# Kernel optimization log

Measured on AMD Instinct MI355X. Metric: run time of the kernel, lower is better.

Reference implementation:

```python
import jax, jax.numpy as jnp
import numpy as np
from jax import lax

N_SRC = 2
K_BASES = 8
N_ITER = 5
NMF_EPS = 1e-20
IP_EPS = 1e-20


def setup_inputs() -> dict:
    key = jax.random.key(0)
    kx, kt, kv = jax.random.split(key, 3)
    M, J, I = 2, 2048, 1025
    X = jax.random.normal(kx, (M, J, I, 2), dtype=jnp.float32)
    T0 = jax.random.uniform(kt, (I, K_BASES, N_SRC), dtype=jnp.float32,
                            minval=1e-08, maxval=1.0)
    V0 = jax.random.uniform(kv, (K_BASES, J, N_SRC), dtype=jnp.float32,
                            minval=1e-08, maxval=1.0)
    return {"X": X, "T0": T0, "V0": V0}


def _nmf_update(Tn, Vn, Yn, eps):
    # Tn: (I,K), Vn: (K,J), Yn: (I,J) complex
    Rn = Tn @ Vn
    magR = jnp.abs(Rn)
    YdR = jnp.abs(Yn) ** 2 / (magR ** 2 + eps)   # |Y|^2 / R^2
    Rd = 1.0 / (magR + eps)
    Tn = Tn * jnp.sqrt((YdR @ Vn.T) / (Rd @ Vn.T + eps))
    Rn = Tn @ Vn
    Rd2 = 1.0 / (jnp.abs(Rn) + eps)
    Vn = Vn * jnp.sqrt((Tn.T @ YdR) / (Tn.T @ Rd2 + eps))
    return Tn, Vn, Tn @ Vn


def _ilrma(X, T0, V0):
    M, J, I, _ = X.shape
    N = N_SRC
    # view_as_complex(X.permute(2,0,1,3)) -> (I, M, J) complex
    Xc = (X[..., 0] + 1j * X[..., 1]).astype(jnp.complex64).transpose(2, 0, 1)
    eye_M = jnp.eye(M, dtype=jnp.complex64)
    W0 = jnp.broadcast_to(jnp.eye(N, M, dtype=jnp.complex64), (I, N, M))
    Y0 = jnp.einsum('inm,imj->inj', W0, Xc)

    def one_iter(carry, _):
        W, T, V, Y = carry
        for n in range(N):  # N=2, structurally distinct small loop
            Tn, Vn, Rn = _nmf_update(T[:, :, n], V[:, :, n], Y[:, n, :], NMF_EPS)
            T = T.at[:, :, n].set(Tn)
            V = V.at[:, :, n].set(Vn)
            # batched per-frequency-bin IP update (vectorizes torch's loop over i)
            inv_Rn = 1.0 / (Rn + IP_EPS)                      # (I,J)
            Xw = Xc * jnp.sqrt(inv_Rn)[:, None, :]            # (I,M,J)
            D = jnp.einsum('imj,ikj->imk', Xw, Xw.conj()) / J  # (I,M,M)
            Dreg = D + IP_EPS * eye_M
            A = jnp.einsum('inm,imk->ink', W, Dreg)           # (I,N,M), N==M
            e_n = eye_M[:, n]                                  # (M,)
            b = jnp.linalg.solve(A, jnp.broadcast_to(e_n, (I, M))[..., None])[..., 0]  # (I,M)
            Db = jnp.einsum('imk,ik->im', Dreg, b)
            denom = jnp.sqrt(jnp.real(jnp.einsum('im,im->i', b.conj(), Db)) + IP_EPS)
            W = W.at[:, n, :].set((b / denom[:, None]).conj())
        Y = jnp.einsum('inm,imj->inj', W, Xc)
        return (W, T, V, Y), None

    (W, T, V, Y), _ = lax.scan(one_iter, (W0, T0, V0, Y0), None, length=N_ITER)
    out = Y.transpose(1, 2, 0)                 # (N, J, I)
    return jnp.stack([out.real, out.imag], axis=-1)  # view_as_real -> (N,J,I,2)


def reference(X, T0, V0):
    return _ilrma(X, T0, V0)
```

## Files before the change

kernel.cpp:

```cpp
#include <hip/hip_runtime.h>

#define I_DIM 1025
#define J_DIM 2048
#define K_B 8
#define IC 33
#define EPSF 1e-20f


__device__ __forceinline__ int rev4i(int x) {
  return ((x & 1) << 3) | ((x & 2) << 1) | ((x & 4) >> 1) | ((x & 8) >> 3);
}

__device__ __forceinline__ void foldReduce16(float* vals, int lane) {
  #pragma unroll
  for (int step = 0; step < 4; ++step) {
    const int nv = 8 >> step;
    const int bit = (lane >> step) & 1;
    #pragma unroll
    for (int q = 0; q < nv; ++q) {
      float a = vals[q], b = vals[q + nv];
      float send = bit ? a : b;
      float keep = bit ? b : a;
      vals[q] = keep + __shfl_xor(send, 1 << step);
    }
  }
  vals[0] += __shfl_xor(vals[0], 16);
  vals[0] += __shfl_xor(vals[0], 32);
}

__device__ __forceinline__ void foldReduce4(float* vals, int lane) {
  #pragma unroll
  for (int step = 0; step < 2; ++step) {
    const int nv = 2 >> step;
    const int bit = (lane >> step) & 1;
    #pragma unroll
    for (int q = 0; q < nv; ++q) {
      float a = vals[q], b = vals[q + nv];
      float send = bit ? a : b;
      float keep = bit ? b : a;
      vals[q] = keep + __shfl_xor(send, 1 << step);
    }
  }
  vals[0] += __shfl_xor(vals[0], 4);
  vals[0] += __shfl_xor(vals[0], 8);
  vals[0] += __shfl_xor(vals[0], 16);
  vals[0] += __shfl_xor(vals[0], 32);
}

__device__ __forceinline__ float2 cmul(float2 a, float2 b) {
  return make_float2(a.x*b.x - a.y*b.y, a.x*b.y + a.y*b.x);
}
__device__ __forceinline__ float2 cadd(float2 a, float2 b) {
  return make_float2(a.x + b.x, a.y + b.y);
}
__device__ __forceinline__ float2 csub(float2 a, float2 b) {
  return make_float2(a.x - b.x, a.y - b.y);
}
__device__ __forceinline__ float2 cdiv(float2 a, float2 b) {
  float s = 1.0f / (b.x*b.x + b.y*b.y);
  return make_float2((a.x*b.x + a.y*b.y)*s, (a.y*b.x - a.x*b.y)*s);
}

__global__ __launch_bounds__(256) void k_tr_init(
    const float* __restrict__ X, float4* __restrict__ Xq,
    const float* __restrict__ T0, const float* __restrict__ V0,
    float* __restrict__ T, float* __restrict__ V, float* __restrict__ W)
{
  const int tx = threadIdx.x, ty = threadIdx.y;
  const int lt = ty * 32 + tx;
  const int bid = blockIdx.y * 33 + blockIdx.x;
  int t = bid * 256 + lt;
  if (t < 2 * K_B * J_DIM) {
    int n = t >> 14;
    int r = t & 16383;
    int j = r >> 3, k = r & 7;
    V[t] = V0[(k * J_DIM + j) * 2 + n];
  }
  if (t < 2 * I_DIM * K_B) {
    int n = t / (I_DIM * K_B);
    int r = t % (I_DIM * K_B);
    int i = r / K_B, k = r % K_B;
    T[t] = T0[(i * K_B + k) * 2 + n];
  }
  if (t < I_DIM * 8) {
    int u = t & 7;
    int c = u & 1, m = (u >> 1) & 1, n = u >> 2;
    W[t] = (n == m && c == 0) ? 1.0f : 0.0f;
  }
  __shared__ float t0r[32][33], t0i[32][33], t1r[32][33], t1i[32][33];
  const int i0 = blockIdx.x * 32, j0 = blockIdx.y * 32;
  const float2* __restrict__ X2 = (const float2*)X;
  #pragma unroll
  for (int jj = 0; jj < 4; ++jj) {
    int jl = ty + jj * 8;
    int i = i0 + tx;
    if (i < I_DIM) {
      float2 v0 = X2[(size_t)(0 * J_DIM + j0 + jl) * I_DIM + i];
      float2 v1 = X2[(size_t)(1 * J_DIM + j0 + jl) * I_DIM + i];
      t0r[jl][tx] = v0.x; t0i[jl][tx] = v0.y;
      t1r[jl][tx] = v1.x; t1i[jl][tx] = v1.y;
    }
  }
  __syncthreads();
  #pragma unroll
  for (int ii = 0; ii < 4; ++ii) {
    int il = ty + ii * 8;
    int i = i0 + il;
    if (i < I_DIM) {
      Xq[(size_t)i * J_DIM + j0 + tx] =
        make_float4(t0r[tx][il], t0i[tx][il], t1r[tx][il], t1i[tx][il]);
    }
  }
}

template<int N>
__device__ __forceinline__ void nmfT_body(
    int i, int tid,
    const float4* __restrict__ Xq,
    float* __restrict__ T, const float* __restrict__ V,
    const float* __restrict__ W, float* __restrict__ YdR)
{
  float4 xs[8];
  #pragma unroll
  for (int u = 0; u < 8; ++u) xs[u] = Xq[(size_t)i * J_DIM + u * 256 + tid];

  const float4 w = ((const float4*)W)[i * 2 + N];
  float t[K_B];
  const int trow = (N * I_DIM + i) * K_B;
  #pragma unroll
  for (int k = 0; k < K_B; ++k) t[k] = T[trow + k];

  float num[K_B], den[K_B];
  #pragma unroll
  for (int k = 0; k < K_B; ++k) { num[k] = 0.f; den[k] = 0.f; }

  const float4* __restrict__ V4 = (const float4*)V;
  #pragma unroll
  for (int u = 0; u < 8; ++u) {
    int j = u * 256 + tid;
    float4 va = V4[(N * J_DIM + j) * 2 + 0];
    float4 vb = V4[(N * J_DIM + j) * 2 + 1];
    float v[K_B] = {va.x, va.y, va.z, va.w, vb.x, vb.y, vb.z, vb.w};
    float rn = 0.f;
    #pragma unroll
    for (int k = 0; k < K_B; ++k) rn += t[k] * v[k];
    float4 x = xs[u];
    float yr = w.x * x.x - w.y * x.y + w.z * x.z - w.w * x.w;
    float yi = w.x * x.y + w.y * x.x + w.z * x.w + w.w * x.z;
    float rd = 1.0f / (fabsf(rn) + EPSF);
    float ydr = (yr * yr + yi * yi) * rd * rd;
    YdR[(size_t)i * J_DIM + j] = ydr;
    #pragma unroll
    for (int k = 0; k < K_B; ++k) { num[k] += ydr * v[k]; den[k] += rd * v[k]; }
  }

  float vals[16];
  #pragma unroll
  for (int k = 0; k < K_B; ++k) { vals[k] = num[k]; vals[K_B + k] = den[k]; }
  const int wave = tid >> 6, lane = tid & 63;
  foldReduce16(vals, lane);
  __shared__ float redT[4][16];
  if (lane < 16) redT[wave][lane] = vals[0];
  __syncthreads();
  if (tid < K_B) {
    int r = rev4i(tid);
    float nm = redT[0][r] + redT[1][r] + redT[2][r] + redT[3][r];
    float dn = redT[0][r+1] + redT[1][r+1] + redT[2][r+1] + redT[3][r+1];
    T[trow + tid] *= sqrtf(nm / (dn + EPSF));
  }
}

template<int N>
__device__ __forceinline__ void ip_solve(
    int i, float D00, float p, float q, float D11, float* __restrict__ W)
{
  D00 += EPSF; D11 += EPSF;
  float2 D01 = make_float2(p, q);
  float2 D10 = make_float2(p, -q);
  float4 w0 = ((const float4*)W)[i * 2 + 0];
  float4 w1 = ((const float4*)W)[i * 2 + 1];
  float2 W00 = make_float2(w0.x, w0.y), W01 = make_float2(w0.z, w0.w);
  float2 W10 = make_float2(w1.x, w1.y), W11 = make_float2(w1.z, w1.w);
  float2 A00 = cadd(make_float2(W00.x * D00, W00.y * D00), cmul(W01, D10));
  float2 A01 = cadd(cmul(W00, D01), make_float2(W01.x * D11, W01.y * D11));
  float2 A10 = cadd(make_float2(W10.x * D00, W10.y * D00), cmul(W11, D10));
  float2 A11 = cadd(cmul(W10, D01), make_float2(W11.x * D11, W11.y * D11));
  float2 det = csub(cmul(A00, A11), cmul(A01, A10));
  float2 b0, b1;
  if (N == 0) {
    b0 = cdiv(A11, det);
    b1 = cdiv(make_float2(-A10.x, -A10.y), det);
  } else {
    b0 = cdiv(make_float2(-A01.x, -A01.y), det);
    b1 = cdiv(A00, det);
  }
  float2 Db0 = cadd(make_float2(D00 * b0.x, D00 * b0.y), cmul(D01, b1));
  float2 Db1 = cadd(cmul(D10, b0), make_float2(D11 * b1.x, D11 * b1.y));
  float ip = b0.x * Db0.x + b0.y * Db0.y + b1.x * Db1.x + b1.y * Db1.y;
  float inv = 1.0f / sqrtf(ip + EPSF);
  ((float4*)W)[i * 2 + N] = make_float4(b0.x * inv, -b0.y * inv, b1.x * inv, -b1.y * inv);
}

template<int N>
__device__ __forceinline__ void ip_body(
    int i, int tid,
    const float4* __restrict__ Xq,
    const float* __restrict__ T, const float* __restrict__ V,
    float* __restrict__ W)
{
  float4 xs[8];
  #pragma unroll
  for (int u = 0; u < 8; ++u) xs[u] = Xq[(size_t)i * J_DIM + u * 256 + tid];

  float t[K_B];
  const int trow = (N * I_DIM + i) * K_B;
  #pragma unroll
  for (int k = 0; k < K_B; ++k) t[k] = T[trow + k];

  const float4* __restrict__ V4 = (const float4*)V;
  float d00 = 0.f, d01r = 0.f, d01i = 0.f, d11 = 0.f;
  #pragma unroll
  for (int u = 0; u < 8; ++u) {
    int j = u * 256 + tid;
    float4 va = V4[(N * J_DIM + j) * 2 + 0];
    float4 vb = V4[(N * J_DIM + j) * 2 + 1];
    float rn = t[0]*va.x + t[1]*va.y + t[2]*va.z + t[3]*va.w
             + t[4]*vb.x + t[5]*vb.y + t[6]*vb.z + t[7]*vb.w;
    float wgt = 1.0f / (rn + EPSF);
    float4 x = xs[u];
    d00 += (x.x * x.x + x.y * x.y) * wgt;
    d11 += (x.z * x.z + x.w * x.w) * wgt;
    d01r += (x.x * x.z + x.y * x.w) * wgt;
    d01i += (x.y * x.z - x.x * x.w) * wgt;
  }
  float vals[4] = {d00, d01r, d01i, d11};
  const int wave = tid >> 6, lane = tid & 63;
  foldReduce4(vals, lane);
  __shared__ float redI[4][4];
  if (lane < 4) redI[wave][lane] = vals[0];
  __syncthreads();
  if (tid == 0) {
    const float invJ = 1.0f / (float)J_DIM;
    float D00 = (redI[0][0] + redI[1][0] + redI[2][0] + redI[3][0]) * invJ;
    float pr  = (redI[0][2] + redI[1][2] + redI[2][2] + redI[3][2]) * invJ;
    float qi  = (redI[0][1] + redI[1][1] + redI[2][1] + redI[3][1]) * invJ;
    float D11 = (redI[0][3] + redI[1][3] + redI[2][3] + redI[3][3]) * invJ;
    ip_solve<N>(i, D00, pr, qi, D11, W);
  }
}

template<int N>
__device__ __forceinline__ void part_body(
    int pb, int tid,
    const float* __restrict__ T, const float* __restrict__ V,
    const float* __restrict__ YdR,
    float* __restrict__ Pn, float* __restrict__ Pd)
{
  const int jb = pb & 7;
  const int c  = pb >> 3;
  const int j  = jb * 256 + tid;
  const int i0 = c * 32;
  const int ni = min(32, I_DIM - i0);
  __shared__ float sT[32 * K_B];
  if (tid < ni * K_B) sT[tid] = T[(N * I_DIM + i0) * K_B + tid];
  __syncthreads();
  const float4* __restrict__ V4 = (const float4*)V;
  float4 va = V4[(N * J_DIM + j) * 2 + 0];
  float4 vb = V4[(N * J_DIM + j) * 2 + 1];
  float v[K_B] = {va.x, va.y, va.z, va.w, vb.x, vb.y, vb.z, vb.w};
  float num[K_B], den[K_B];
  #pragma unroll
  for (int k = 0; k < K_B; ++k) { num[k] = 0.f; den[k] = 0.f; }

  if (ni == 32) {
    #pragma unroll
    for (int g = 0; g < 4; ++g) {
      float yd[8];
      #pragma unroll
      for (int q = 0; q < 8; ++q)
        yd[q] = YdR[(size_t)(i0 + g * 8 + q) * J_DIM + j];
      #pragma unroll
      for (int q = 0; q < 8; ++q) {
        const int ii = g * 8 + q;
        float rn = 0.f;
        #pragma unroll
        for (int k = 0; k < K_B; ++k) rn += sT[ii * K_B + k] * v[k];
        float rd2 = 1.0f / (fabsf(rn) + EPSF);
        #pragma unroll
        for (int k = 0; k < K_B; ++k) {
          num[k] += sT[ii * K_B + k] * yd[q];
          den[k] += sT[ii * K_B + k] * rd2;
        }
      }
    }
  } else {
    for (int ii = 0; ii < ni; ++ii) {
      float ydr = YdR[(size_t)(i0 + ii) * J_DIM + j];
      float rn = 0.f;
      #pragma unroll
      for (int k = 0; k < K_B; ++k) rn += sT[ii * K_B + k] * v[k];
      float rd2 = 1.0f / (fabsf(rn) + EPSF);
      #pragma unroll
      for (int k = 0; k < K_B; ++k) {
        num[k] += sT[ii * K_B + k] * ydr;
        den[k] += sT[ii * K_B + k] * rd2;
      }
    }
  }
  ((float4*)Pn)[((size_t)c * J_DIM + j) * 2 + 0] = make_float4(num[0], num[1], num[2], num[3]);
  ((float4*)Pn)[((size_t)c * J_DIM + j) * 2 + 1] = make_float4(num[4], num[5], num[6], num[7]);
  ((float4*)Pd)[((size_t)c * J_DIM + j) * 2 + 0] = make_float4(den[0], den[1], den[2], den[3]);
  ((float4*)Pd)[((size_t)c * J_DIM + j) * 2 + 1] = make_float4(den[4], den[5], den[6], den[7]);
}

template<int N>
__device__ __forceinline__ void fin_body(
    int fb, int tid, float* __restrict__ V,
    const float* __restrict__ Pn, const float* __restrict__ Pd)
{
  const int t = fb * 256 + tid;
  float nm = 0.f, dn = 0.f;
  #pragma unroll
  for (int c = 0; c < IC; ++c) {
    nm += Pn[(size_t)c * (K_B * J_DIM) + t];
    dn += Pd[(size_t)c * (K_B * J_DIM) + t];
  }
  V[N * (K_B * J_DIM) + t] *= sqrtf(nm / (dn + EPSF));
}

template<int NT, int NP>
__global__ __launch_bounds__(256) void k_s2(
    const float4* __restrict__ Xq, float* __restrict__ T,
    const float* __restrict__ V, const float* __restrict__ W,
    float* __restrict__ YdR_t, const float* __restrict__ YdR_p,
    float* __restrict__ Pn, float* __restrict__ Pd)
{
  if (blockIdx.x < 264)
    part_body<NP>(blockIdx.x, threadIdx.x, T, V, YdR_p, Pn, Pd);
  else
    nmfT_body<NT>(blockIdx.x - 264, threadIdx.x, Xq, T, V, W, YdR_t);
}

template<int NF, int NP>
__global__ __launch_bounds__(256) void k_s3(
    float* __restrict__ V,
    const float* __restrict__ Pn_f, const float* __restrict__ Pd_f,
    const float* __restrict__ T, const float* __restrict__ YdR_p,
    float* __restrict__ Pn_p, float* __restrict__ Pd_p)
{
  if (blockIdx.x < 64)
    fin_body<NF>(blockIdx.x, threadIdx.x, V, Pn_f, Pd_f);
  else
    part_body<NP>(blockIdx.x - 64, threadIdx.x, T, V, YdR_p, Pn_p, Pd_p);
}

template<int NI, int NF>
__global__ __launch_bounds__(256) void k_s4(
    const float4* __restrict__ Xq, const float* __restrict__ T,
    float* __restrict__ V, float* __restrict__ W,
    const float* __restrict__ Pn_f, const float* __restrict__ Pd_f)
{
  if (blockIdx.x < 64)
    fin_body<NF>(blockIdx.x, threadIdx.x, V, Pn_f, Pd_f);
  else
    ip_body<NI>(blockIdx.x - 64, threadIdx.x, Xq, T, V, W);
}

template<int NT, int NI>
__global__ __launch_bounds__(256) void k_s1(
    const float4* __restrict__ Xq, float* __restrict__ T,
    const float* __restrict__ V, float* __restrict__ W,
    float* __restrict__ YdR_t)
{
  int b = blockIdx.x;
  int p, pop;
  if (b >= 2048) { p = 1024; pop = b - 2048; }
  else { pop = (b >> 3) & 1; p = ((b >> 4) << 3) | (b & 7); }
  if (pop == 0)
    ip_body<NI>(p, threadIdx.x, Xq, T, V, W);
  else
    nmfT_body<NT>(p, threadIdx.x, Xq, T, V, W, YdR_t);
}

template<int N>
__global__ __launch_bounds__(256) void k_nmfT(
    const float4* __restrict__ Xq, float* __restrict__ T,
    const float* __restrict__ V, const float* __restrict__ W,
    float* __restrict__ YdR)
{
  nmfT_body<N>(blockIdx.x, threadIdx.x, Xq, T, V, W, YdR);
}

template<int N>
__global__ __launch_bounds__(256) void k_ip(
    const float4* __restrict__ Xq, const float* __restrict__ T,
    const float* __restrict__ V, float* __restrict__ W)
{
  ip_body<N>(blockIdx.x, threadIdx.x, Xq, T, V, W);
}

__global__ __launch_bounds__(256) void k_out(
    const float* __restrict__ X, const float* __restrict__ W, float* __restrict__ out)
{
  const int j = blockIdx.x;
  const int i = blockIdx.y * 256 + threadIdx.x;
  if (i >= I_DIM) return;
  const float2* __restrict__ X2 = (const float2*)X;
  float2 x0 = X2[(size_t)(0 * J_DIM + j) * I_DIM + i];
  float2 x1 = X2[(size_t)(1 * J_DIM + j) * I_DIM + i];
  const float4* __restrict__ W4 = (const float4*)W;
  float4 w0 = W4[i * 2 + 0];
  float4 w1 = W4[i * 2 + 1];
  float2* __restrict__ O = (float2*)out;
  float yr = w0.x * x0.x - w0.y * x0.y + w0.z * x1.x - w0.w * x1.y;
  float yi = w0.x * x0.y + w0.y * x0.x + w0.z * x1.y + w0.w * x1.x;
  O[(size_t)(0 * J_DIM + j) * I_DIM + i] = make_float2(yr, yi);
  yr = w1.x * x0.x - w1.y * x0.y + w1.z * x1.x - w1.w * x1.y;
  yi = w1.x * x0.y + w1.y * x0.x + w1.z * x1.y + w1.w * x1.x;
  O[(size_t)(1 * J_DIM + j) * I_DIM + i] = make_float2(yr, yi);
}

extern "C" void kernel_launch(void* const* d_in, const int* in_sizes, int n_in,
                              void* d_out, int out_size, void* d_ws, size_t ws_size,
                              hipStream_t stream) {
  const float* X  = (const float*)d_in[0];
  const float* T0 = (const float*)d_in[1];
  const float* V0 = (const float*)d_in[2];
  float* ws = (float*)d_ws;
  float4* Xq  = (float4*)ws;
  float* YdR0 = ws + 8396800;
  float* YdR1 = ws + 10496000;
  float* T    = ws + 12595200;
  float* V    = ws + 12611600;
  float* W    = ws + 12644368;
  float* Pn0  = ws + 12652568;
  float* Pd0  = ws + 13193240;
  float* Pn1  = ws + 13733912;
  float* Pd1  = ws + 14274584;
  float* out  = (float*)d_out;

  k_tr_init<<<dim3(33, 64), dim3(32, 8), 0, stream>>>(X, Xq, T0, V0, T, V, W);
  k_nmfT<0><<<I_DIM, 256, 0, stream>>>(Xq, T, V, W, YdR0);
  for (int it = 0; it < 5; ++it) {
    k_s2<1, 0><<<264 + I_DIM, 256, 0, stream>>>(Xq, T, V, W, YdR1, YdR0, Pn0, Pd0);
    k_s3<0, 1><<<64 + 264, 256, 0, stream>>>(V, Pn0, Pd0, T, YdR1, Pn1, Pd1);
    k_s4<0, 1><<<64 + I_DIM, 256, 0, stream>>>(Xq, T, V, W, Pn1, Pd1);
    if (it < 4) {
      k_s1<0, 1><<<2 * I_DIM, 256, 0, stream>>>(Xq, T, V, W, YdR0);
    } else {
      k_ip<1><<<I_DIM, 256, 0, stream>>>(Xq, T, V, W);
    }
  }
  k_out<<<dim3(J_DIM, 5), 256, 0, stream>>>(X, W, out);
}
```

Measured before the change: 313.4 us.

## Batch both sources per stage and fuse the two IP updates into one kernel

The staggered per-source pipeline, which interleaved the NMF, partial-sum, finalize and IP stages of sources 0 and 1 across launches, is replaced by one stage-per-kernel schedule handling both sources together. The IP kernel now loads X once per frequency bin, accumulates the weighted covariance for both sources, and solves both W rows sequentially in one thread. This removes a second full pass over X per iteration and the separate initial NMF launch. In exchange it loses the overlap between stages of different sources, and the partial-sum and finalize launches now have small grids that may underfill the GPU.

```diff
diff --git a/kernel.cpp b/kernel.cpp
--- a/kernel.cpp
+++ b/kernel.cpp
@@ -10,6 +10,9 @@
 __device__ __forceinline__ int rev4i(int x) {
   return ((x & 1) << 3) | ((x & 2) << 1) | ((x & 4) >> 1) | ((x & 8) >> 3);
 }
+__device__ __forceinline__ int rev3i(int x) {
+  return ((x & 1) << 2) | (x & 2) | ((x & 4) >> 2);
+}
 
 __device__ __forceinline__ void foldReduce16(float* vals, int lane) {
   #pragma unroll
@@ -28,10 +31,10 @@
   vals[0] += __shfl_xor(vals[0], 32);
 }
 
-__device__ __forceinline__ void foldReduce4(float* vals, int lane) {
-  #pragma unroll
-  for (int step = 0; step < 2; ++step) {
-    const int nv = 2 >> step;
+__device__ __forceinline__ void foldReduce8(float* vals, int lane) {
+  #pragma unroll
+  for (int step = 0; step < 3; ++step) {
+    const int nv = 4 >> step;
     const int bit = (lane >> step) & 1;
     #pragma unroll
     for (int q = 0; q < nv; ++q) {
@@ -41,7 +44,6 @@
       vals[q] = keep + __shfl_xor(send, 1 << step);
     }
   }
-  vals[0] += __shfl_xor(vals[0], 4);
   vals[0] += __shfl_xor(vals[0], 8);
   vals[0] += __shfl_xor(vals[0], 16);
   vals[0] += __shfl_xor(vals[0], 32);
@@ -170,83 +172,54 @@
   }
 }
 
-template<int N>
-__device__ __forceinline__ void ip_solve(
-    int i, float D00, float p, float q, float D11, float* __restrict__ W)
-{
-  D00 += EPSF; D11 += EPSF;
-  float2 D01 = make_float2(p, q);
-  float2 D10 = make_float2(p, -q);
+__device__ __forceinline__ void ip_solve_both(
+    int i,
+    float D000, float p0, float q0, float D110,
+    float D001, float p1, float q1, float D111,
+    float* __restrict__ W)
+{
   float4 w0 = ((const float4*)W)[i * 2 + 0];
   float4 w1 = ((const float4*)W)[i * 2 + 1];
   float2 W00 = make_float2(w0.x, w0.y), W01 = make_float2(w0.z, w0.w);
   float2 W10 = make_float2(w1.x, w1.y), W11 = make_float2(w1.z, w1.w);
-  float2 A00 = cadd(make_float2(W00.x * D00, W00.y * D00), cmul(W01, D10));
-  float2 A01 = cadd(cmul(W00, D01), make_float2(W01.x * D11, W01.y * D11));
-  float2 A10 = cadd(make_float2(W10.x * D00, W10.y * D00), cmul(W11, D10));
-  float2 A11 = cadd(cmul(W10, D01), make_float2(W11.x * D11, W11.y * D11));
-  float2 det = csub(cmul(A00, A11), cmul(A01, A10));
-  float2 b0, b1;
-  if (N == 0) {
-    b0 = cdiv(A11, det);
-    b1 = cdiv(make_float2(-A10.x, -A10.y), det);
-  } else {
-    b0 = cdiv(make_float2(-A01.x, -A01.y), det);
-    b1 = cdiv(A00, det);
-  }
-  float2 Db0 = cadd(make_float2(D00 * b0.x, D00 * b0.y), cmul(D01, b1));
-  float2 Db1 = cadd(cmul(D10, b0), make_float2(D11 * b1.x, D11 * b1.y));
-  float ip = b0.x * Db0.x + b0.y * Db0.y + b1.x * Db1.x + b1.y * Db1.y;
-  float inv = 1.0f / sqrtf(ip + EPSF);
-  ((float4*)W)[i * 2 + N] = make_float4(b0.x * inv, -b0.y * inv, b1.x * inv, -b1.y * inv);
-}
-
-template<int N>
-__device__ __forceinline__ void ip_body(
-    int i, int tid,
-    const float4* __restrict__ Xq,
-    const float* __restrict__ T, const float* __restrict__ V,
-    float* __restrict__ W)
-{
-  float4 xs[8];
-  #pragma unroll
-  for (int u = 0; u < 8; ++u) xs[u] = Xq[(size_t)i * J_DIM + u * 256 + tid];
-
-  float t[K_B];
-  const int trow = (N * I_DIM + i) * K_B;
-  #pragma unroll
-  for (int k = 0; k < K_B; ++k) t[k] = T[trow + k];
-
-  const float4* __restrict__ V4 = (const float4*)V;
-  float d00 = 0.f, d01r = 0.f, d01i = 0.f, d11 = 0.f;
-  #pragma unroll
-  for (int u = 0; u < 8; ++u) {
-    int j = u * 256 + tid;
-    float4 va = V4[(N * J_DIM + j) * 2 + 0];
-    float4 vb = V4[(N * J_DIM + j) * 2 + 1];
-    float rn = t[0]*va.x + t[1]*va.y + t[2]*va.z + t[3]*va.w
-             + t[4]*vb.x + t[5]*vb.y + t[6]*vb.z + t[7]*vb.w;
-    float wgt = 1.0f / (rn + EPSF);
-    float4 x = xs[u];
-    d00 += (x.x * x.x + x.y * x.y) * wgt;
-    d11 += (x.z * x.z + x.w * x.w) * wgt;
-    d01r += (x.x * x.z + x.y * x.w) * wgt;
-    d01i += (x.y * x.z - x.x * x.w) * wgt;
-  }
-  float vals[4] = {d00, d01r, d01i, d11};
-  const int wave = tid >> 6, lane = tid & 63;
-  foldReduce4(vals, lane);
-  __shared__ float redI[4][4];
-  if (lane < 4) redI[wave][lane] = vals[0];
-  __syncthreads();
-  if (tid == 0) {
-    const float invJ = 1.0f / (float)J_DIM;
-    float D00 = (redI[0][0] + redI[1][0] + redI[2][0] + redI[3][0]) * invJ;
-    float pr  = (redI[0][2] + redI[1][2] + redI[2][2] + redI[3][2]) * invJ;
-    float qi  = (redI[0][1] + redI[1][1] + redI[2][1] + redI[3][1]) * invJ;
-    float D11 = (redI[0][3] + redI[1][3] + redI[2][3] + redI[3][3]) * invJ;
-    ip_solve<N>(i, D00, pr, qi, D11, W);
-  }
+  {
+    float D00 = D000 + EPSF, D11 = D110 + EPSF;
+    float2 D01 = make_float2(p0, q0);
+    float2 D10 = make_float2(p0, -q0);
+    float2 A00 = cadd(make_float2(W00.x * D00, W00.y * D00), cmul(W01, D10));
+    float2 A01 = cadd(cmul(W00, D01), make_float2(W01.x * D11, W01.y * D11));
+    float2 A10 = cadd(make_float2(W10.x * D00, W10.y * D00), cmul(W11, D10));
+    float2 A11 = cadd(cmul(W10, D01), make_float2(W11.x * D11, W11.y * D11));
+    float2 det = csub(cmul(A00, A11), cmul(A01, A10));
+    float2 b0 = cdiv(A11, det);
+    float2 b1 = cdiv(make_float2(-A10.x, -A10.y), det);
+    float2 Db0 = cadd(make_float2(D00 * b0.x, D00 * b0.y), cmul(D01, b1));
+    float2 Db1 = cadd(cmul(D10, b0), make_float2(D11 * b1.x, D11 * b1.y));
+    float ip = b0.x * Db0.x + b0.y * Db0.y + b1.x * Db1.x + b1.y * Db1.y;
+    float inv = 1.0f / sqrtf(ip + EPSF);
+    W00 = make_float2(b0.x * inv, -b0.y * inv);
+    W01 = make_float2(b1.x * inv, -b1.y * inv);
+  }
+  {
+    float D00 = D001 + EPSF, D11 = D111 + EPSF;
+    float2 D01 = make_float2(p1, q1);
+    float2 D10 = make_float2(p1, -q1);
+    float2 A00 = cadd(make_float2(W00.x * D00, W00.y * D00), cmul(W01, D10));
+    float2 A01 = cadd(cmul(W00, D01), make_float2(W01.x * D11, W01.y * D11));
+    float2 A10 = cadd(make_float2(W10.x * D00, W10.y * D00), cmul(W11, D10));
+    float2 A11 = cadd(cmul(W10, D01), make_float2(W11.x * D11, W11.y * D11));
+    float2 det = csub(cmul(A00, A11), cmul(A01, A10));
+    float2 b0 = cdiv(make_float2(-A01.x, -A01.y), det);
+    float2 b1 = cdiv(A00, det);
+    float2 Db0 = cadd(make_float2(D00 * b0.x, D00 * b0.y), cmul(D01, b1));
+    float2 Db1 = cadd(cmul(D10, b0), make_float2(D11 * b1.x, D11 * b1.y));
+    float ip = b0.x * Db0.x + b0.y * Db0.y + b1.x * Db1.x + b1.y * Db1.y;
+    float inv = 1.0f / sqrtf(ip + EPSF);
+    W10 = make_float2(b0.x * inv, -b0.y * inv);
+    W11 = make_float2(b1.x * inv, -b1.y * inv);
+  }
+  ((float4*)W)[i * 2 + 0] = make_float4(W00.x, W00.y, W01.x, W01.y);
+  ((float4*)W)[i * 2 + 1] = make_float4(W10.x, W10.y, W11.x, W11.y);
 }
 
 template<int N>
@@ -328,75 +301,101 @@
   V[N * (K_B * J_DIM) + t] *= sqrtf(nm / (dn + EPSF));
 }
 
-template<int NT, int NP>
-__global__ __launch_bounds__(256) void k_s2(
+__global__ __launch_bounds__(256) void k_nmf2(
     const float4* __restrict__ Xq, float* __restrict__ T,
     const float* __restrict__ V, const float* __restrict__ W,
-    float* __restrict__ YdR_t, const float* __restrict__ YdR_p,
-    float* __restrict__ Pn, float* __restrict__ Pd)
-{
-  if (blockIdx.x < 264)
-    part_body<NP>(blockIdx.x, threadIdx.x, T, V, YdR_p, Pn, Pd);
-  else
-    nmfT_body<NT>(blockIdx.x - 264, threadIdx.x, Xq, T, V, W, YdR_t);
-}
-
-template<int NF, int NP>
-__global__ __launch_bounds__(256) void k_s3(
-    float* __restrict__ V,
-    const float* __restrict__ Pn_f, const float* __restrict__ Pd_f,
-    const float* __restrict__ T, const float* __restrict__ YdR_p,
-    float* __restrict__ Pn_p, float* __restrict__ Pd_p)
-{
-  if (blockIdx.x < 64)
-    fin_body<NF>(blockIdx.x, threadIdx.x, V, Pn_f, Pd_f);
-  else
-    part_body<NP>(blockIdx.x - 64, threadIdx.x, T, V, YdR_p, Pn_p, Pd_p);
-}
-
-template<int NI, int NF>
-__global__ __launch_bounds__(256) void k_s4(
-    const float4* __restrict__ Xq, const float* __restrict__ T,
-    float* __restrict__ V, float* __restrict__ W,
-    const float* __restrict__ Pn_f, const float* __restrict__ Pd_f)
-{
-  if (blockIdx.x < 64)
-    fin_body<NF>(blockIdx.x, threadIdx.x, V, Pn_f, Pd_f);
-  else
-    ip_body<NI>(blockIdx.x - 64, threadIdx.x, Xq, T, V, W);
-}
-
-template<int NT, int NI>
-__global__ __launch_bounds__(256) void k_s1(
-    const float4* __restrict__ Xq, float* __restrict__ T,
-    const float* __restrict__ V, float* __restrict__ W,
-    float* __restrict__ YdR_t)
+    float* __restrict__ YdR0, float* __restrict__ YdR1)
 {
   int b = blockIdx.x;
   int p, pop;
   if (b >= 2048) { p = 1024; pop = b - 2048; }
   else { pop = (b >> 3) & 1; p = ((b >> 4) << 3) | (b & 7); }
   if (pop == 0)
-    ip_body<NI>(p, threadIdx.x, Xq, T, V, W);
+    nmfT_body<0>(p, threadIdx.x, Xq, T, V, W, YdR0);
   else
-    nmfT_body<NT>(p, threadIdx.x, Xq, T, V, W, YdR_t);
-}
-
-template<int N>
-__global__ __launch_bounds__(256) void k_nmfT(
-    const float4* __restrict__ Xq, float* __restrict__ T,
-    const float* __restrict__ V, const float* __restrict__ W,
-    float* __restrict__ YdR)
-{
-  nmfT_body<N>(blockIdx.x, threadIdx.x, Xq, T, V, W, YdR);
-}
-
-template<int N>
-__global__ __launch_bounds__(256) void k_ip(
+    nmfT_body<1>(p, threadIdx.x, Xq, T, V, W, YdR1);
+}
+
+__global__ __launch_bounds__(256) void k_part2(
+    const float* __restrict__ T, const float* __restrict__ V,
+    const float* __restrict__ Y0, const float* __restrict__ Y1,
+    float* __restrict__ Pn0, float* __restrict__ Pd0,
+    float* __restrict__ Pn1, float* __restrict__ Pd1)
+{
+  if (blockIdx.x < 264)
+    part_body<0>(blockIdx.x, threadIdx.x, T, V, Y0, Pn0, Pd0);
+  else
+    part_body<1>(blockIdx.x - 264, threadIdx.x, T, V, Y1, Pn1, Pd1);
+}
+
+__global__ __launch_bounds__(256) void k_fin2(
+    float* __restrict__ V,
+    const float* __restrict__ Pn0, const float* __restrict__ Pd0,
+    const float* __restrict__ Pn1, const float* __restrict__ Pd1)
+{
+  if (blockIdx.x < 64)
+    fin_body<0>(blockIdx.x, threadIdx.x, V, Pn0, Pd0);
+  else
+    fin_body<1>(blockIdx.x - 64, threadIdx.x, V, Pn1, Pd1);
+}
+
+__global__ __launch_bounds__(256) void k_ip2(
     const float4* __restrict__ Xq, const float* __restrict__ T,
     const float* __restrict__ V, float* __restrict__ W)
 {
-  ip_body<N>(blockIdx.x, threadIdx.x, Xq, T, V, W);
+  const int i = blockIdx.x;
+  const int tid = threadIdx.x;
+  float4 xs[8];
+  #pragma unroll
+  for (int u = 0; u < 8; ++u) xs[u] = Xq[(size_t)i * J_DIM + u * 256 + tid];
+
+  float t0[K_B], t1[K_B];
+  #pragma unroll
+  for (int k = 0; k < K_B; ++k) {
+    t0[k] = T[(0 * I_DIM + i) * K_B + k];
+    t1[k] = T[(1 * I_DIM + i) * K_B + k];
+  }
+  const float4* __restrict__ V4 = (const float4*)V;
+  float acc[8];
+  #pragma unroll
+  for (int q = 0; q < 8; ++q) acc[q] = 0.f;
+
+  #pragma unroll
+  for (int u = 0; u < 8; ++u) {
+    int j = u * 256 + tid;
+    float4 va0 = V4[(0 * J_DIM + j) * 2 + 0];
+    float4 vb0 = V4[(0 * J_DIM + j) * 2 + 1];
+    float4 va1 = V4[(1 * J_DIM + j) * 2 + 0];
+    float4 vb1 = V4[(1 * J_DIM + j) * 2 + 1];
+    float rn0 = t0[0]*va0.x + t0[1]*va0.y + t0[2]*va0.z + t0[3]*va0.w
+              + t0[4]*vb0.x + t0[5]*vb0.y + t0[6]*vb0.z + t0[7]*vb0.w;
+    float rn1 = t1[0]*va1.x + t1[1]*va1.y + t1[2]*va1.z + t1[3]*va1.w
+              + t1[4]*vb1.x + t1[5]*vb1.y + t1[6]*vb1.z + t1[7]*vb1.w;
+    float w0 = 1.0f / (rn0 + EPSF);
+    float w1 = 1.0f / (rn1 + EPSF);
+    float4 x = xs[u];
+    float m00 = x.x * x.x + x.y * x.y;
+    float m11 = x.z * x.z + x.w * x.w;
+    float m01r = x.x * x.z + x.y * x.w;
+    float m01i = x.y * x.z - x.x * x.w;
+    acc[0] += m00 * w0; acc[1] += m01r * w0; acc[2] += m01i * w0; acc[3] += m11 * w0;
+    acc[4] += m00 * w1; acc[5] += m01r * w1; acc[6] += m01i * w1; acc[7] += m11 * w1;
+  }
+  const int wave = tid >> 6, lane = tid & 63;
+  foldReduce8(acc, lane);
+  __shared__ float red[4][8];
+  if (lane < 8) red[wave][lane] = acc[0];
+  __syncthreads();
+  if (tid == 0) {
+    const float invJ = 1.0f / (float)J_DIM;
+    float s[8];
+    #pragma unroll
+    for (int vv = 0; vv < 8; ++vv) {
+      int r = rev3i(vv);
+      s[vv] = (red[0][r] + red[1][r] + red[2][r] + red[3][r]) * invJ;
+    }
+    ip_solve_both(i, s[0], s[1], s[2], s[3], s[4], s[5], s[6], s[7], W);
+  }
 }
 
 __global__ __launch_bounds__(256) void k_out(
@@ -440,16 +439,11 @@
   float* out  = (float*)d_out;
 
   k_tr_init<<<dim3(33, 64), dim3(32, 8), 0, stream>>>(X, Xq, T0, V0, T, V, W);
-  k_nmfT<0><<<I_DIM, 256, 0, stream>>>(Xq, T, V, W, YdR0);
   for (int it = 0; it < 5; ++it) {
-    k_s2<1, 0><<<264 + I_DIM, 256, 0, stream>>>(Xq, T, V, W, YdR1, YdR0, Pn0, Pd0);
-    k_s3<0, 1><<<64 + 264, 256, 0, stream>>>(V, Pn0, Pd0, T, YdR1, Pn1, Pd1);
-    k_s4<0, 1><<<64 + I_DIM, 256, 0, stream>>>(Xq, T, V, W, Pn1, Pd1);
-    if (it < 4) {
-      k_s1<0, 1><<<2 * I_DIM, 256, 0, stream>>>(Xq, T, V, W, YdR0);
-    } else {
-      k_ip<1><<<I_DIM, 256, 0, stream>>>(Xq, T, V, W);
-    }
+    k_nmf2<<<2 * I_DIM, 256, 0, stream>>>(Xq, T, V, W, YdR0, YdR1);
+    k_part2<<<2 * 264, 256, 0, stream>>>(T, V, YdR0, YdR1, Pn0, Pd0, Pn1, Pd1);
+    k_fin2<<<2 * 64, 256, 0, stream>>>(V, Pn0, Pd0, Pn1, Pd1);
+    k_ip2<<<I_DIM, 256, 0, stream>>>(Xq, T, V, W);
   }
   k_out<<<dim3(J_DIM, 5), 256, 0, stream>>>(X, W, out);
 }
```

Measured after the change: 292.8 us. -6.6%, faster.
